# Optimization experiments

Measured on AMD Instinct MI355X. Metric: run time of the kernel, lower is better.

The kernel has to match this reference:

```python
import jax, jax.numpy as jnp
import numpy as np
from jax.scipy.special import logsumexp

EPS = 0.05        # entropic regularization (Sinkhorn approximation of exact LP WMD)
N_ITERS = 200     # Sinkhorn iterations


def setup_inputs() -> dict:
    key = jax.random.key(0)
    k1, k2, k3 = jax.random.split(key, 3)
    B, M, N, D = 64, 512, 512, 128
    x = jax.random.normal(k1, (B, M, D), dtype=jnp.float32)
    y = jax.random.normal(k2, (B, N, D), dtype=jnp.float32)
    labels = jax.random.uniform(k3, (B,), dtype=jnp.float32)
    return {"x": x, "y": y, "labels": labels}


def _cost_matrix(x, y):
    # D[b,i,j] = sqrt(mean_d (x[b,i]-y[b,j])^2), computed without the [B,M,N,D] intermediate
    d = x.shape[-1]
    xn = jnp.sum(x * x, axis=-1)                       # [B,M]
    yn = jnp.sum(y * y, axis=-1)                       # [B,N]
    xy = jnp.einsum('bmd,bnd->bmn', x, y)              # [B,M,N]
    sq = (xn[:, :, None] + yn[:, None, :] - 2.0 * xy) / d
    return jnp.sqrt(jnp.maximum(sq, 1e-12))


def _sinkhorn_wmd(D):
    # uniform marginals p=1/M, q=1/N; log-domain Sinkhorn
    B, M, N = D.shape
    logp = -jnp.log(jnp.float32(M))
    logq = -jnp.log(jnp.float32(N))
    f0 = jnp.zeros((B, M), D.dtype)
    g0 = jnp.zeros((B, N), D.dtype)

    def step(carry, _):
        f, g = carry
        f = EPS * (logp - logsumexp((g[:, None, :] - D) / EPS, axis=2))  # [B,M]
        g = EPS * (logq - logsumexp((f[:, :, None] - D) / EPS, axis=1))  # [B,N]
        return (f, g), None

    (f, g), _ = jax.lax.scan(step, (f0, g0), None, length=N_ITERS)
    P = jnp.exp((f[:, :, None] + g[:, None, :] - D) / EPS)  # transport plan [B,M,N]
    return jnp.sum(P * D, axis=(1, 2))                      # WMD per sample [B]


def reference(x, y, labels):
    D = _cost_matrix(x, y)
    wmd = _sinkhorn_wmd(D)          # per-sample Word Mover's Distance
    return jnp.mean((wmd - labels) ** 2)  # MSELoss
```

## Files before the change

### kernel.cpp

```cpp
#include <hip/hip_runtime.h>
#include <hip/hip_fp16.h>

#define B_ 64
#define M_ 512
#define N_ 512
#define D_ 128
constexpr float EPS_ = 0.05f;
constexpr float SHIFT_ = 1.0f;
constexpr int NIT_ = 200;

typedef _Float16 h2 __attribute__((ext_vector_type(2)));

__device__ __forceinline__ h2 u2h(unsigned x) { return __builtin_bit_cast(h2, x); }
__device__ __forceinline__ unsigned h2u(h2 x) { return __builtin_bit_cast(unsigned, x); }

__device__ __forceinline__ float fdot2_(h2 a, h2 b, float c) {
#if __has_builtin(__builtin_amdgcn_fdot2)
    return __builtin_amdgcn_fdot2(a, b, c, false);
#else
    float2 af = __half22float2(__builtin_bit_cast(__half2, a));
    float2 bf = __half22float2(__builtin_bit_cast(__half2, b));
    return fmaf(af.x, bf.x, fmaf(af.y, bf.y, c));
#endif
}

__global__ __launch_bounds__(256) void wmd_norms(const float* __restrict__ x,
                                                 const float* __restrict__ y,
                                                 float* __restrict__ xn,
                                                 float* __restrict__ yn) {
    int gw = (int)((blockIdx.x * blockDim.x + threadIdx.x) >> 6);
    int l = threadIdx.x & 63;
    const float* src; float* dst; int row;
    if (gw < B_ * M_) { src = x; dst = xn; row = gw; }
    else              { src = y; dst = yn; row = gw - B_ * M_; }
    float2 a = ((const float2*)(src + (size_t)row * D_))[l];
    float s = a.x * a.x + a.y * a.y;
#pragma unroll
    for (int off = 32; off; off >>= 1) s += __shfl_xor(s, off);
    if (l == 0) dst[row] = s;
}

__global__ __launch_bounds__(256) void wmd_build_k(const float* __restrict__ x,
                                                   const float* __restrict__ y,
                                                   const float* __restrict__ xn,
                                                   const float* __restrict__ yn,
                                                   __half* __restrict__ Kp) {
    int b = blockIdx.z, it = blockIdx.y, jt = blockIdx.x;
    __shared__ float xs[32][129];
    __shared__ float ys[32][129];
    const float4* xb = (const float4*)(x + ((size_t)b * M_ + it * 32) * D_);
    const float4* yb = (const float4*)(y + ((size_t)b * N_ + jt * 32) * D_);
    int t = threadIdx.x;
#pragma unroll
    for (int k = 0; k < 4; ++k) {
        int idx = t + k * 256;
        int r = idx >> 5, c = (idx & 31) * 4;
        float4 vx = xb[idx];
        float4 vy = yb[idx];
        xs[r][c] = vx.x; xs[r][c + 1] = vx.y; xs[r][c + 2] = vx.z; xs[r][c + 3] = vx.w;
        ys[r][c] = vy.x; ys[r][c + 1] = vy.y; ys[r][c + 2] = vy.z; ys[r][c + 3] = vy.w;
    }
    __syncthreads();
    int ti = t >> 5, tj = t & 31;
    float a0 = 0.f, a1 = 0.f, a2 = 0.f, a3 = 0.f;
    for (int d = 0; d < D_; ++d) {
        float yv = ys[tj][d];
        a0 += xs[ti][d] * yv;
        a1 += xs[ti + 8][d] * yv;
        a2 += xs[ti + 16][d] * yv;
        a3 += xs[ti + 24][d] * yv;
    }
    float ynj = yn[(size_t)b * N_ + jt * 32 + tj];
    float accs[4] = {a0, a1, a2, a3};
#pragma unroll
    for (int k = 0; k < 4; ++k) {
        int gi = it * 32 + ti + 8 * k;
        float sq = (xn[(size_t)b * M_ + gi] + ynj - 2.0f * accs[k]) * (1.0f / D_);
        float Dv = sqrtf(fmaxf(sq, 1e-12f));
        float kv = expf((SHIFT_ - Dv) * (1.0f / EPS_));
        kv = fmaxf(kv, 1e-7f);
        Kp[((size_t)b * M_ + gi) * N_ + jt * 32 + tj] = __float2half(kv);
    }
}

__global__ __launch_bounds__(1024, 4) void wmd_sinkhorn(const __half* __restrict__ K,
                                                        float* __restrict__ wmd) {
    int b = blockIdx.x;
    const __half* Kb = K + (size_t)b * M_ * N_;
    __shared__ __half mrg[16][N_];
    __shared__ __half v_sh[N_];
    __shared__ float u_s[M_];
    __shared__ float wsum[16];
    int t = threadIdx.x, w = t >> 6, l = t & 63;
    int sub = l & 15, rg = l >> 4;
    const float pmarg = 1.0f / M_, qmarg = 1.0f / N_;

    h2 vh[16];
    _Float16 one = (_Float16)1.0f;
#pragma unroll
    for (int j = 0; j < 16; ++j) vh[j] = (h2){one, one};

#pragma unroll 1
    for (int it = 0; it < NIT_; ++it) {
        h2 ca[16];
        _Float16 z = (_Float16)0.0f;
#pragma unroll
        for (int j = 0; j < 16; ++j) ca[j] = (h2){z, z};

#pragma unroll 2
        for (int g = 0; g < 8; ++g) {
            int row = (w << 5) + (g << 2) + rg;
            const __half* rp = Kb + (size_t)row * N_ + sub * 8;
            uint4 kq[4];
#pragma unroll
            for (int c = 0; c < 4; ++c) kq[c] = *(const uint4*)(rp + 128 * c);
            const unsigned* kk = (const unsigned*)kq;
            float d0 = 0.f, d1 = 0.f, d2 = 0.f, d3 = 0.f;
#pragma unroll
            for (int j = 0; j < 4; ++j) {
                d0 = fdot2_(u2h(kk[j]),      vh[j],      d0);
                d1 = fdot2_(u2h(kk[4 + j]),  vh[4 + j],  d1);
                d2 = fdot2_(u2h(kk[8 + j]),  vh[8 + j],  d2);
                d3 = fdot2_(u2h(kk[12 + j]), vh[12 + j], d3);
            }
            float dot = (d0 + d1) + (d2 + d3);
#pragma unroll
            for (int off = 1; off < 16; off <<= 1) dot += __shfl_xor(dot, off);
            float u = pmarg * __builtin_amdgcn_rcpf(dot);
            if (sub == 0) u_s[row] = u;
            _Float16 uf = (_Float16)u;
            h2 uh = (h2){uf, uf};
#pragma unroll
            for (int j = 0; j < 16; ++j) ca[j] = u2h(kk[j]) * uh + ca[j];
        }
#pragma unroll
        for (int j = 0; j < 16; ++j) {
            ca[j] = ca[j] + u2h((unsigned)__shfl_xor((int)h2u(ca[j]), 16));
            ca[j] = ca[j] + u2h((unsigned)__shfl_xor((int)h2u(ca[j]), 32));
        }
        if (l < 16) {
#pragma unroll
            for (int c = 0; c < 4; ++c) {
                uint4 pk = {h2u(ca[4 * c]), h2u(ca[4 * c + 1]),
                            h2u(ca[4 * c + 2]), h2u(ca[4 * c + 3])};
                *(uint4*)&mrg[w][sub * 8 + 128 * c] = pk;
            }
        }
        __syncthreads();
        if (t < N_) {
            float s = 0.f;
#pragma unroll
            for (int ww = 0; ww < 16; ++ww) s += __half2float(mrg[ww][t]);
            v_sh[t] = __float2half_rn(qmarg * __builtin_amdgcn_rcpf(s));
        }
        __syncthreads();
#pragma unroll
        for (int c = 0; c < 4; ++c) {
            uint4 vv = *(const uint4*)&v_sh[sub * 8 + 128 * c];
            vh[4 * c]     = u2h(vv.x);
            vh[4 * c + 1] = u2h(vv.y);
            vh[4 * c + 2] = u2h(vv.z);
            vh[4 * c + 3] = u2h(vv.w);
        }
    }

    float acc = 0.f;
#pragma unroll 1
    for (int g = 0; g < 8; ++g) {
        int row = (w << 5) + (g << 2) + rg;
        const __half* rp = Kb + (size_t)row * N_ + sub * 8;
        float u = u_s[row];
#pragma unroll
        for (int c = 0; c < 4; ++c) {
            uint4 kq = *(const uint4*)(rp + 128 * c);
            const unsigned* kk = (const unsigned*)&kq;
#pragma unroll
            for (int j = 0; j < 4; ++j) {
                float2 kf = __half22float2(__builtin_bit_cast(__half2, kk[j]));
                float2 vf = __half22float2(__builtin_bit_cast(__half2, h2u(vh[4 * c + j])));
                acc += (u * kf.x * vf.x) * (SHIFT_ - EPS_ * __logf(kf.x));
                acc += (u * kf.y * vf.y) * (SHIFT_ - EPS_ * __logf(kf.y));
            }
        }
    }
#pragma unroll
    for (int off = 1; off < 64; off <<= 1) acc += __shfl_xor(acc, off);
    if (l == 0) wsum[w] = acc;
    __syncthreads();
    if (t == 0) {
        float s = 0.f;
#pragma unroll
        for (int ww = 0; ww < 16; ++ww) s += wsum[ww];
        wmd[b] = s;
    }
}

__global__ void wmd_mse(const float* __restrict__ wmd, const float* __restrict__ labels,
                        float* __restrict__ out) {
    int l = threadIdx.x;
    float d = wmd[l] - labels[l];
    d = d * d;
#pragma unroll
    for (int off = 32; off; off >>= 1) d += __shfl_xor(d, off);
    if (l == 0) out[0] = d * (1.0f / B_);
}

extern "C" void kernel_launch(void* const* d_in, const int* in_sizes, int n_in,
                              void* d_out, int out_size, void* d_ws, size_t ws_size,
                              hipStream_t stream) {
    const float* x = (const float*)d_in[0];
    const float* y = (const float*)d_in[1];
    const float* labels = (const float*)d_in[2];
    float* out = (float*)d_out;

    char* ws = (char*)d_ws;
    __half* K = (__half*)ws;
    size_t off = (size_t)B_ * M_ * N_ * sizeof(__half);
    float* xn = (float*)(ws + off);        off += (size_t)B_ * M_ * sizeof(float);
    float* yn = (float*)(ws + off);        off += (size_t)B_ * N_ * sizeof(float);
    float* wmd = (float*)(ws + off);

    wmd_norms<<<(B_ * (M_ + N_)) / 4, 256, 0, stream>>>(x, y, xn, yn);
    wmd_build_k<<<dim3(N_ / 32, M_ / 32, B_), 256, 0, stream>>>(x, y, xn, yn, K);
    wmd_sinkhorn<<<B_, 1024, 0, stream>>>(K, wmd);
    wmd_mse<<<1, 64, 0, stream>>>(wmd, labels, out);
}
```

Baseline: 1.404 ms.

## Store Gibbs kernel in FP8 and keep it register-resident across Sinkhorn iterations

```diff
diff --git a/kernel.cpp b/kernel.cpp
--- a/kernel.cpp
+++ b/kernel.cpp
@@ -6,22 +6,39 @@
 #define N_ 512
 #define D_ 128
 constexpr float EPS_ = 0.05f;
-constexpr float SHIFT_ = 1.0f;
+constexpr float SHIFT_ = 1.25f;
 constexpr int NIT_ = 200;
 
 typedef _Float16 h2 __attribute__((ext_vector_type(2)));
-
+typedef float f2 __attribute__((ext_vector_type(2)));
+
+__device__ __forceinline__ unsigned h2u(h2 x) { return __builtin_bit_cast(unsigned, x); }
 __device__ __forceinline__ h2 u2h(unsigned x) { return __builtin_bit_cast(h2, x); }
-__device__ __forceinline__ unsigned h2u(h2 x) { return __builtin_bit_cast(unsigned, x); }
-
-__device__ __forceinline__ float fdot2_(h2 a, h2 b, float c) {
+
+template <bool HI>
+__device__ __forceinline__ h2 cvt_h2(unsigned w) {
+    f2 f = __builtin_amdgcn_cvt_pk_f32_fp8((int)w, HI);
+    return __builtin_bit_cast(h2, __builtin_amdgcn_cvt_pkrtz(f.x, f.y));
+}
+template <bool HI>
+__device__ __forceinline__ f2 cvt_f2(unsigned w) {
+    return __builtin_amdgcn_cvt_pk_f32_fp8((int)w, HI);
+}
+
+__device__ __forceinline__ float dot2f(h2 a, h2 b, float c) {
 #if __has_builtin(__builtin_amdgcn_fdot2)
     return __builtin_amdgcn_fdot2(a, b, c, false);
 #else
-    float2 af = __half22float2(__builtin_bit_cast(__half2, a));
-    float2 bf = __half22float2(__builtin_bit_cast(__half2, b));
-    return fmaf(af.x, bf.x, fmaf(af.y, bf.y, c));
+    return fmaf((float)a.x, (float)b.x, fmaf((float)a.y, (float)b.y, c));
 #endif
+}
+
+__device__ __forceinline__ float red16(float x) {
+    x += __builtin_bit_cast(float, __builtin_amdgcn_mov_dpp(__builtin_bit_cast(int, x), 0xB1, 0xF, 0xF, true));
+    x += __builtin_bit_cast(float, __builtin_amdgcn_mov_dpp(__builtin_bit_cast(int, x), 0x4E, 0xF, 0xF, true));
+    x += __builtin_bit_cast(float, __builtin_amdgcn_mov_dpp(__builtin_bit_cast(int, x), 0x124, 0xF, 0xF, true));
+    x += __builtin_bit_cast(float, __builtin_amdgcn_mov_dpp(__builtin_bit_cast(int, x), 0x128, 0xF, 0xF, true));
+    return x;
 }
 
 __global__ __launch_bounds__(256) void wmd_norms(const float* __restrict__ x,
@@ -44,7 +61,7 @@
                                                    const float* __restrict__ y,
                                                    const float* __restrict__ xn,
                                                    const float* __restrict__ yn,
-                                                   __half* __restrict__ Kp) {
+                                                   unsigned char* __restrict__ Kp) {
     int b = blockIdx.z, it = blockIdx.y, jt = blockIdx.x;
     __shared__ float xs[32][129];
     __shared__ float ys[32][129];
@@ -77,25 +94,35 @@
         int gi = it * 32 + ti + 8 * k;
         float sq = (xn[(size_t)b * M_ + gi] + ynj - 2.0f * accs[k]) * (1.0f / D_);
         float Dv = sqrtf(fmaxf(sq, 1e-12f));
-        float kv = expf((SHIFT_ - Dv) * (1.0f / EPS_));
-        kv = fmaxf(kv, 1e-7f);
-        Kp[((size_t)b * M_ + gi) * N_ + jt * 32 + tj] = __float2half(kv);
-    }
-}
-
-__global__ __launch_bounds__(1024, 4) void wmd_sinkhorn(const __half* __restrict__ K,
+        float kv = fminf(expf((SHIFT_ - Dv) * (1.0f / EPS_)), 448.0f);
+        unsigned r8 = (unsigned)__builtin_amdgcn_cvt_pk_fp8_f32(kv, kv, 0, false);
+        Kp[((size_t)b * M_ + gi) * N_ + jt * 32 + tj] = (unsigned char)(r8 & 0xff);
+    }
+}
+
+__global__ __launch_bounds__(1024, 4) void wmd_sinkhorn(const unsigned char* __restrict__ K8,
                                                         float* __restrict__ wmd) {
     int b = blockIdx.x;
-    const __half* Kb = K + (size_t)b * M_ * N_;
-    __shared__ __half mrg[16][N_];
-    __shared__ __half v_sh[N_];
-    __shared__ float u_s[M_];
+    const unsigned char* Kb = K8 + (size_t)b * M_ * N_;
+    __shared__ h2 mrg[64][264];
+    __shared__ h2 v_sh[256];
     __shared__ float wsum[16];
     int t = threadIdx.x, w = t >> 6, l = t & 63;
     int sub = l & 15, rg = l >> 4;
-    const float pmarg = 1.0f / M_, qmarg = 1.0f / N_;
+    const float pmarg = 1.0f / M_;
+
+    uint2 kr[32];
+    {
+        const unsigned char* base = Kb + ((size_t)(w * 32 + rg) * N_) + sub * 8;
+#pragma unroll
+        for (int g = 0; g < 8; ++g)
+#pragma unroll
+            for (int c = 0; c < 4; ++c)
+                kr[g * 4 + c] = *(const uint2*)(base + g * 4 * N_ + c * 128);
+    }
 
     h2 vh[16];
+    float u_f[8];
     _Float16 one = (_Float16)1.0f;
 #pragma unroll
     for (int j = 0; j < 16; ++j) vh[j] = (h2){one, one};
@@ -107,57 +134,64 @@
 #pragma unroll
         for (int j = 0; j < 16; ++j) ca[j] = (h2){z, z};
 
-#pragma unroll 2
+#pragma unroll
         for (int g = 0; g < 8; ++g) {
-            int row = (w << 5) + (g << 2) + rg;
-            const __half* rp = Kb + (size_t)row * N_ + sub * 8;
-            uint4 kq[4];
-#pragma unroll
-            for (int c = 0; c < 4; ++c) kq[c] = *(const uint4*)(rp + 128 * c);
-            const unsigned* kk = (const unsigned*)kq;
             float d0 = 0.f, d1 = 0.f, d2 = 0.f, d3 = 0.f;
 #pragma unroll
-            for (int j = 0; j < 4; ++j) {
-                d0 = fdot2_(u2h(kk[j]),      vh[j],      d0);
-                d1 = fdot2_(u2h(kk[4 + j]),  vh[4 + j],  d1);
-                d2 = fdot2_(u2h(kk[8 + j]),  vh[8 + j],  d2);
-                d3 = fdot2_(u2h(kk[12 + j]), vh[12 + j], d3);
-            }
-            float dot = (d0 + d1) + (d2 + d3);
-#pragma unroll
-            for (int off = 1; off < 16; off <<= 1) dot += __shfl_xor(dot, off);
-            float u = pmarg * __builtin_amdgcn_rcpf(dot);
-            if (sub == 0) u_s[row] = u;
-            _Float16 uf = (_Float16)u;
+            for (int c = 0; c < 4; ++c) {
+                unsigned lo = kr[g * 4 + c].x, hi = kr[g * 4 + c].y;
+                d0 = dot2f(cvt_h2<false>(lo), vh[4 * c + 0], d0);
+                d1 = dot2f(cvt_h2<true>(lo),  vh[4 * c + 1], d1);
+                d2 = dot2f(cvt_h2<false>(hi), vh[4 * c + 2], d2);
+                d3 = dot2f(cvt_h2<true>(hi),  vh[4 * c + 3], d3);
+            }
+            float dot = red16((d0 + d1) + (d2 + d3));
+            float rd = __builtin_amdgcn_rcpf(dot);
+            u_f[g] = rd;
+            _Float16 uf = (_Float16)rd;
             h2 uh = (h2){uf, uf};
 #pragma unroll
-            for (int j = 0; j < 16; ++j) ca[j] = u2h(kk[j]) * uh + ca[j];
-        }
-#pragma unroll
-        for (int j = 0; j < 16; ++j) {
-            ca[j] = ca[j] + u2h((unsigned)__shfl_xor((int)h2u(ca[j]), 16));
-            ca[j] = ca[j] + u2h((unsigned)__shfl_xor((int)h2u(ca[j]), 32));
-        }
-        if (l < 16) {
-#pragma unroll
             for (int c = 0; c < 4; ++c) {
-                uint4 pk = {h2u(ca[4 * c]), h2u(ca[4 * c + 1]),
-                            h2u(ca[4 * c + 2]), h2u(ca[4 * c + 3])};
-                *(uint4*)&mrg[w][sub * 8 + 128 * c] = pk;
-            }
+                unsigned lo = kr[g * 4 + c].x, hi = kr[g * 4 + c].y;
+                ca[4 * c + 0] = cvt_h2<false>(lo) * uh + ca[4 * c + 0];
+                ca[4 * c + 1] = cvt_h2<true>(lo)  * uh + ca[4 * c + 1];
+                ca[4 * c + 2] = cvt_h2<false>(hi) * uh + ca[4 * c + 2];
+                ca[4 * c + 3] = cvt_h2<true>(hi)  * uh + ca[4 * c + 3];
+            }
+        }
+        int mr = (w << 2) + rg;
+#pragma unroll
+        for (int c = 0; c < 4; ++c) {
+            uint4 pk = {h2u(ca[4 * c]), h2u(ca[4 * c + 1]), h2u(ca[4 * c + 2]), h2u(ca[4 * c + 3])};
+            *(uint4*)&mrg[mr][sub * 4 + 64 * c] = pk;
         }
         __syncthreads();
-        if (t < N_) {
-            float s = 0.f;
-#pragma unroll
-            for (int ww = 0; ww < 16; ++ww) s += __half2float(mrg[ww][t]);
-            v_sh[t] = __float2half_rn(qmarg * __builtin_amdgcn_rcpf(s));
+        {
+            int part = rg, cc = sub;
+            int col2 = (w << 4) + cc;
+            h2 s0 = (h2){z, z}, s1 = (h2){z, z}, s2 = (h2){z, z}, s3 = (h2){z, z};
+#pragma unroll
+            for (int k = 0; k < 4; ++k) {
+                s0 = s0 + mrg[4 * (4 * k + 0) + part][col2];
+                s1 = s1 + mrg[4 * (4 * k + 1) + part][col2];
+                s2 = s2 + mrg[4 * (4 * k + 2) + part][col2];
+                s3 = s3 + mrg[4 * (4 * k + 3) + part][col2];
+            }
+            h2 s = (s0 + s1) + (s2 + s3);
+            s = s + u2h((unsigned)__builtin_amdgcn_ds_swizzle((int)h2u(s), 0x401F));
+            s = s + u2h((unsigned)__shfl_xor((int)h2u(s), 32));
+            if (l < 16) {
+                h2 vv;
+                vv.x = (_Float16)__builtin_amdgcn_rcpf((float)s.x);
+                vv.y = (_Float16)__builtin_amdgcn_rcpf((float)s.y);
+                v_sh[col2] = vv;
+            }
         }
         __syncthreads();
 #pragma unroll
         for (int c = 0; c < 4; ++c) {
-            uint4 vv = *(const uint4*)&v_sh[sub * 8 + 128 * c];
-            vh[4 * c]     = u2h(vv.x);
+            uint4 vv = *(const uint4*)&v_sh[sub * 4 + 64 * c];
+            vh[4 * c + 0] = u2h(vv.x);
             vh[4 * c + 1] = u2h(vv.y);
             vh[4 * c + 2] = u2h(vv.z);
             vh[4 * c + 3] = u2h(vv.w);
@@ -165,21 +199,19 @@
     }
 
     float acc = 0.f;
-#pragma unroll 1
+#pragma unroll
     for (int g = 0; g < 8; ++g) {
-        int row = (w << 5) + (g << 2) + rg;
-        const __half* rp = Kb + (size_t)row * N_ + sub * 8;
-        float u = u_s[row];
+        float us = u_f[g];
 #pragma unroll
         for (int c = 0; c < 4; ++c) {
-            uint4 kq = *(const uint4*)(rp + 128 * c);
-            const unsigned* kk = (const unsigned*)&kq;
+            unsigned lo = kr[g * 4 + c].x, hi = kr[g * 4 + c].y;
+            f2 kp[4] = {cvt_f2<false>(lo), cvt_f2<true>(lo), cvt_f2<false>(hi), cvt_f2<true>(hi)};
 #pragma unroll
             for (int j = 0; j < 4; ++j) {
-                float2 kf = __half22float2(__builtin_bit_cast(__half2, kk[j]));
-                float2 vf = __half22float2(__builtin_bit_cast(__half2, h2u(vh[4 * c + j])));
-                acc += (u * kf.x * vf.x) * (SHIFT_ - EPS_ * __logf(kf.x));
-                acc += (u * kf.y * vf.y) * (SHIFT_ - EPS_ * __logf(kf.y));
+                h2 vhj = vh[4 * c + j];
+                float kx = fmaxf(kp[j].x, 1e-9f), ky = fmaxf(kp[j].y, 1e-9f);
+                acc += (us * kx * (float)vhj.x) * (SHIFT_ - EPS_ * __logf(kx));
+                acc += (us * ky * (float)vhj.y) * (SHIFT_ - EPS_ * __logf(ky));
             }
         }
     }
@@ -191,7 +223,7 @@
         float s = 0.f;
 #pragma unroll
         for (int ww = 0; ww < 16; ++ww) s += wsum[ww];
-        wmd[b] = s;
+        wmd[b] = s * pmarg;
     }
 }
 
@@ -214,14 +246,14 @@
     float* out = (float*)d_out;
 
     char* ws = (char*)d_ws;
-    __half* K = (__half*)ws;
-    size_t off = (size_t)B_ * M_ * N_ * sizeof(__half);
+    unsigned char* K8 = (unsigned char*)ws;
+    size_t off = (size_t)B_ * M_ * N_;
     float* xn = (float*)(ws + off);        off += (size_t)B_ * M_ * sizeof(float);
     float* yn = (float*)(ws + off);        off += (size_t)B_ * N_ * sizeof(float);
     float* wmd = (float*)(ws + off);
 
     wmd_norms<<<(B_ * (M_ + N_)) / 4, 256, 0, stream>>>(x, y, xn, yn);
-    wmd_build_k<<<dim3(N_ / 32, M_ / 32, B_), 256, 0, stream>>>(x, y, xn, yn, K);
-    wmd_sinkhorn<<<B_, 1024, 0, stream>>>(K, wmd);
+    wmd_build_k<<<dim3(N_ / 32, M_ / 32, B_), 256, 0, stream>>>(x, y, xn, yn, K8);
+    wmd_sinkhorn<<<B_, 1024, 0, stream>>>(K8, wmd);
     wmd_mse<<<1, 64, 0, stream>>>(wmd, labels, out);
 }
```

After: 1.271 ms. 1.1x faster.
